# Performance work log

Hardware: AMD Instinct MI355X
Metric: run time of the kernel (lower is better)

The kernel has to match this reference:

```python
import jax, jax.numpy as jnp
import numpy as np

N_NODES = 50000
N_EDGES = 800000
IN_DIM = 64
HID_DIM = 128
OUT_DIM = 64
BN_EPS = 1e-5


def _glorot(key, shape):
    fan_in, fan_out = shape[0], shape[1]
    lim = (6.0 / (fan_in + fan_out)) ** 0.5
    return jax.random.uniform(key, shape, jnp.float32, -lim, lim)


def setup_inputs() -> dict:
    key = jax.random.key(0)
    ks = jax.random.split(key, 8)
    x = jax.random.normal(ks[0], (N_NODES, IN_DIM), jnp.float32)
    edge_index = jax.random.randint(ks[1], (2, N_EDGES), 0, N_NODES, jnp.int32)
    return {
        "x": x,
        "edge_index": edge_index,
        # SAGEConv1: lin_l (applied to aggregated neighbors, has bias), lin_r (root, no bias)
        "W1l": _glorot(ks[2], (IN_DIM, HID_DIM)),
        "b1": jnp.zeros((HID_DIM,), jnp.float32),
        "W1r": _glorot(ks[3], (IN_DIM, HID_DIM)),
        # BatchNorm1d params
        "gamma": jnp.ones((HID_DIM,), jnp.float32),
        "beta": jnp.zeros((HID_DIM,), jnp.float32),
        # SAGEConv2
        "W2l": _glorot(ks[4], (HID_DIM, OUT_DIM)),
        "b2": jnp.zeros((OUT_DIM,), jnp.float32),
        "W2r": _glorot(ks[5], (HID_DIM, OUT_DIM)),
    }


def _sage_conv(h, src, dst, Wl, b, Wr, deg_inv):
    # mean-aggregate neighbor features per destination node
    agg = jax.ops.segment_sum(h[src], dst, num_segments=N_NODES)  # [N, d]
    agg = agg * deg_inv[:, None]
    return agg @ Wl + b + h @ Wr


def reference(x, edge_index, W1l, b1, W1r, gamma, beta, W2l, b2, W2r):
    src, dst = edge_index[0], edge_index[1]
    deg = jax.ops.segment_sum(jnp.ones((N_EDGES,), jnp.float32), dst,
                              num_segments=N_NODES)
    deg_inv = jnp.where(deg > 0, 1.0 / jnp.maximum(deg, 1.0), 0.0)

    h = _sage_conv(x, src, dst, W1l, b1, W1r, deg_inv)  # [N, hid]
    # BatchNorm1d (training mode: batch stats over nodes, biased variance)
    mu = jnp.mean(h, axis=0)
    var = jnp.mean((h - mu) ** 2, axis=0)
    h = (h - mu) * jax.lax.rsqrt(var + BN_EPS) * gamma + beta
    h = jax.nn.relu(h)
    out = _sage_conv(h, src, dst, W2l, b2, W2r, deg_inv)  # [N, out]
    return out
```

## Files before the change

kernel.cpp:

```cpp
#include <hip/hip_runtime.h>

#define NN 50000
#define NE 800000
#define HID 128
#define OUTD 64
#define NBK 782
#define BWID 64
#define CAP 1264
#define TILE_E 4096
#define XB 3125
#define HB 196

typedef __attribute__((ext_vector_type(8))) short bf16x8;
typedef __attribute__((ext_vector_type(4))) float f32x4;

static __device__ __forceinline__ unsigned short f2bf(float f) {
    unsigned u = __float_as_uint(f);
    unsigned r = (u + 0x7FFFu + ((u >> 16) & 1u)) >> 16;
    return (unsigned short)r;
}
static __device__ __forceinline__ float bflo(unsigned u) { return __uint_as_float(u << 16); }
static __device__ __forceinline__ float bfhi(unsigned u) { return __uint_as_float(u & 0xffff0000u); }

__global__ __launch_bounds__(256) void prep_bin_kernel(
    const float* __restrict__ x, unsigned short* __restrict__ A1,
    const float* __restrict__ W1l, const float* __restrict__ W1r,
    const float* __restrict__ W2l, const float* __restrict__ W2r,
    unsigned short* __restrict__ BT1, unsigned short* __restrict__ BT2,
    const int* __restrict__ src, const int* __restrict__ dst,
    int* __restrict__ gcur, int2* __restrict__ pairs)
{
    __shared__ int lcnt[NBK];
    __shared__ int lbase[NBK];
    int blk = blockIdx.x, tid = threadIdx.x;
    if (blk >= HB) {
        int b2 = blk - HB;
        if (b2 < XB) {
            int idx = b2 * 256 + tid;
            int n = idx >> 4, q = idx & 15;
            float4 v = ((const float4*)x)[idx];
            ushort4 o;
            o.x = f2bf(v.x); o.y = f2bf(v.y); o.z = f2bf(v.z); o.w = f2bf(v.w);
            *(ushort4*)(A1 + (size_t)n * 128 + 64 + q * 4) = o;
        } else {
            int idx = (b2 - XB) * 256 + tid;
            int j = idx >> 7, k = idx & 127;
            float v1 = (k < 64) ? W1l[k * HID + j] : W1r[(k - 64) * HID + j];
            BT1[j * 128 + k] = f2bf(v1);
            float v2 = (j < 64) ? W2l[k * OUTD + j] : W2r[k * OUTD + (j - 64)];
            BT2[j * 128 + k] = f2bf(v2);
        }
        return;
    }
    int e0 = blk * TILE_E;
    for (int i = tid; i < NBK; i += 256) lcnt[i] = 0;
    __syncthreads();
    int s[16], d[16], loc[16];
#pragma unroll
    for (int i = 0; i < 16; i++) {
        int e = e0 + i * 256 + tid;
        if (e < NE) {
            s[i] = __builtin_nontemporal_load(&src[e]);
            d[i] = __builtin_nontemporal_load(&dst[e]);
            loc[i] = atomicAdd(&lcnt[d[i] >> 6], 1);
        }
    }
    __syncthreads();
    for (int b = tid; b < NBK; b += 256)
        lbase[b] = b * CAP + atomicAdd(&gcur[b], lcnt[b]);
    __syncthreads();
#pragma unroll
    for (int i = 0; i < 16; i++) {
        int e = e0 + i * 256 + tid;
        if (e < NE)
            pairs[lbase[d[i] >> 6] + loc[i]] = make_int2(s[i], d[i]);
    }
}

template<int MODE>
__global__ __launch_bounds__(256) void bin_agg_kernel(
    const int2* __restrict__ pairs, const int* __restrict__ gcur,
    const unsigned short* __restrict__ feat, int fstride, int foff,
    unsigned short* __restrict__ outb, int ostride, int ooff,
    float* __restrict__ outf)
{
    __shared__ int lcnt[BWID];
    __shared__ int startL[BWID];
    __shared__ int degL[BWID];
    __shared__ int lcur[BWID];
    __shared__ int permL[CAP];
    int b = blockIdx.x, tid = threadIdx.x;
    int lo = b * CAP;
    int cnt = gcur[b];
    int base = b * BWID;
    if (tid < BWID) lcnt[tid] = 0;
    __syncthreads();
    for (int i = tid; i < cnt; i += 256)
        atomicAdd(&lcnt[pairs[lo + i].y - base], 1);
    __syncthreads();
    if (tid < BWID) {
        int v = lcnt[tid];
        int s = v;
#pragma unroll
        for (int off = 1; off < BWID; off <<= 1) {
            int t = __shfl_up(s, off, 64);
            if (tid >= off) s += t;
        }
        startL[tid] = s - v;
        degL[tid] = v;
        lcur[tid] = s - v;
    }
    __syncthreads();
    for (int i = tid; i < cnt; i += 256) {
        int2 p = pairs[lo + i];
        int pos = atomicAdd(&lcur[p.y - base], 1);
        permL[pos] = p.x;
    }
    __syncthreads();
    int lane = tid & 63, w = tid >> 6;
    int g = lane >> 3;
    int q = lane & 7;
    const unsigned short* fbase = feat + foff + q * 8;
#pragma unroll
    for (int rnd = 0; rnd < 2; rnd++) {
        int nloc = w * 16 + rnd * 8 + g;
        int node = base + nloc;
        int rs = startL[nloc];
        int deg = degL[nloc];
        float acc[8];
#pragma unroll
        for (int t = 0; t < 8; t++) acc[t] = 0.f;
        int i = 0;
        for (; i + 3 < deg; i += 4) {
            int s0 = permL[rs + i];
            int s1 = permL[rs + i + 1];
            int s2 = permL[rs + i + 2];
            int s3 = permL[rs + i + 3];
            uint4 v0 = *(const uint4*)(fbase + (size_t)s0 * fstride);
            uint4 v1 = *(const uint4*)(fbase + (size_t)s1 * fstride);
            uint4 v2 = *(const uint4*)(fbase + (size_t)s2 * fstride);
            uint4 v3 = *(const uint4*)(fbase + (size_t)s3 * fstride);
            acc[0] += bflo(v0.x); acc[1] += bfhi(v0.x);
            acc[2] += bflo(v0.y); acc[3] += bfhi(v0.y);
            acc[4] += bflo(v0.z); acc[5] += bfhi(v0.z);
            acc[6] += bflo(v0.w); acc[7] += bfhi(v0.w);
            acc[0] += bflo(v1.x); acc[1] += bfhi(v1.x);
            acc[2] += bflo(v1.y); acc[3] += bfhi(v1.y);
            acc[4] += bflo(v1.z); acc[5] += bfhi(v1.z);
            acc[6] += bflo(v1.w); acc[7] += bfhi(v1.w);
            acc[0] += bflo(v2.x); acc[1] += bfhi(v2.x);
            acc[2] += bflo(v2.y); acc[3] += bfhi(v2.y);
            acc[4] += bflo(v2.z); acc[5] += bfhi(v2.z);
            acc[6] += bflo(v2.w); acc[7] += bfhi(v2.w);
            acc[0] += bflo(v3.x); acc[1] += bfhi(v3.x);
            acc[2] += bflo(v3.y); acc[3] += bfhi(v3.y);
            acc[4] += bflo(v3.z); acc[5] += bfhi(v3.z);
            acc[6] += bflo(v3.w); acc[7] += bfhi(v3.w);
        }
        for (; i < deg; i++) {
            int s0 = permL[rs + i];
            uint4 v0 = *(const uint4*)(fbase + (size_t)s0 * fstride);
            acc[0] += bflo(v0.x); acc[1] += bfhi(v0.x);
            acc[2] += bflo(v0.y); acc[3] += bfhi(v0.y);
            acc[4] += bflo(v0.z); acc[5] += bfhi(v0.z);
            acc[6] += bflo(v0.w); acc[7] += bfhi(v0.w);
        }
        if (node < NN) {
            float inv = (deg > 0) ? (1.0f / (float)deg) : 0.f;
            if (MODE == 0) {
                uint4 o;
                o.x = (unsigned)f2bf(acc[0] * inv) | ((unsigned)f2bf(acc[1] * inv) << 16);
                o.y = (unsigned)f2bf(acc[2] * inv) | ((unsigned)f2bf(acc[3] * inv) << 16);
                o.z = (unsigned)f2bf(acc[4] * inv) | ((unsigned)f2bf(acc[5] * inv) << 16);
                o.w = (unsigned)f2bf(acc[6] * inv) | ((unsigned)f2bf(acc[7] * inv) << 16);
                *(uint4*)(outb + (size_t)node * ostride + ooff + q * 8) = o;
            } else {
                float4* op = (float4*)(outf + (size_t)node * 64 + q * 8);
                float4 o0 = op[0], o1 = op[1];
                o0.x += acc[0] * inv; o0.y += acc[1] * inv;
                o0.z += acc[2] * inv; o0.w += acc[3] * inv;
                o1.x += acc[4] * inv; o1.y += acc[5] * inv;
                o1.z += acc[6] * inv; o1.w += acc[7] * inv;
                op[0] = o0; op[1] = o1;
            }
        }
    }
}

static __device__ __forceinline__ bf16x8 bnrelu8(uint4 v, const float* sc,
                                                 const float* sh, int j0) {
    float f[8];
    f[0] = bflo(v.x); f[1] = bfhi(v.x);
    f[2] = bflo(v.y); f[3] = bfhi(v.y);
    f[4] = bflo(v.z); f[5] = bfhi(v.z);
    f[6] = bflo(v.w); f[7] = bfhi(v.w);
    unsigned r01, r23, r45, r67;
#pragma unroll
    for (int t = 0; t < 8; t++) {
        float h = f[t] * sc[j0 + t] + sh[j0 + t];
        f[t] = h > 0.f ? h : 0.f;
    }
    r01 = (unsigned)f2bf(f[0]) | ((unsigned)f2bf(f[1]) << 16);
    r23 = (unsigned)f2bf(f[2]) | ((unsigned)f2bf(f[3]) << 16);
    r45 = (unsigned)f2bf(f[4]) | ((unsigned)f2bf(f[5]) << 16);
    r67 = (unsigned)f2bf(f[6]) | ((unsigned)f2bf(f[7]) << 16);
    uint4 o = make_uint4(r01, r23, r45, r67);
    return *(bf16x8*)&o;
}

template<bool IS1>
__global__ __launch_bounds__(256) void conv_mfma_kernel(
    const unsigned short* __restrict__ A, const unsigned short* __restrict__ BT,
    const float* __restrict__ bias,
    unsigned short* __restrict__ outb, float* __restrict__ outf,
    float* __restrict__ sums, float* __restrict__ sumsq,
    const float* __restrict__ gamma, const float* __restrict__ beta)
{
    __shared__ float red_s[4][128];
    __shared__ float red_q[4][128];
    __shared__ float sc[128], sh[128];
    int tid = threadIdx.x;
    int wid = tid >> 6, lane = tid & 63;
    int nl = lane & 15, ko = lane >> 4;
    if (!IS1) {
        if (tid < 128) {
            float inv_n = 1.0f / (float)NN;
            float mu = sums[tid] * inv_n;
            float var = sumsq[tid] * inv_n - mu * mu;
            float s = gamma[tid] * rsqrtf(var + 1e-5f);
            sc[tid] = s;
            sh[tid] = beta[tid] - mu * s;
        }
        __syncthreads();
    }
    int gw = blockIdx.x * 4 + wid;
    int jh = gw & 1;
    int tstride = (gridDim.x * 4) >> 1;
    const int tiles = NN / 16;
    bf16x8 b[4][4];
    const unsigned short* bbase = BT + (size_t)(jh * 64 + nl) * 128 + ko * 8;
#pragma unroll
    for (int jg = 0; jg < 4; jg++)
#pragma unroll
        for (int ks = 0; ks < 4; ks++)
            b[jg][ks] = *(const bf16x8*)(bbase + jg * 16 * 128 + ks * 32);
    float4 bias4[4];
#pragma unroll
    for (int jg = 0; jg < 4; jg++) {
        if (IS1)        bias4[jg] = *(const float4*)(bias + jh * 64 + jg * 16 + ko * 4);
        else if (jh)    bias4[jg] = *(const float4*)(bias + jg * 16 + ko * 4);
        else            bias4[jg] = make_float4(0.f, 0.f, 0.f, 0.f);
    }
    float s_sum[16], s_sq[16];
#pragma unroll
    for (int t = 0; t < 16; t++) { s_sum[t] = 0.f; s_sq[t] = 0.f; }
    int tile = gw >> 1;
    uint4 a[4];
    if (tile < tiles) {
        const unsigned short* arow = A + (size_t)(tile * 16 + nl) * 128 + ko * 8;
#pragma unroll
        for (int ks = 0; ks < 4; ks++) a[ks] = *(const uint4*)(arow + ks * 32);
    }
    while (tile < tiles) {
        int nxt = tile + tstride;
        uint4 an[4];
        if (nxt < tiles) {
            const unsigned short* arow = A + (size_t)(nxt * 16 + nl) * 128 + ko * 8;
#pragma unroll
            for (int ks = 0; ks < 4; ks++) an[ks] = *(const uint4*)(arow + ks * 32);
        }
        bf16x8 af[4];
#pragma unroll
        for (int ks = 0; ks < 4; ks++) {
            if (IS1) af[ks] = *(bf16x8*)&a[ks];
            else     af[ks] = bnrelu8(a[ks], sc, sh, ks * 32 + ko * 8);
        }
        int n_g = tile * 16 + nl;
#pragma unroll
        for (int jg = 0; jg < 4; jg++) {
            f32x4 acc = {0.f, 0.f, 0.f, 0.f};
#pragma unroll
            for (int ks = 0; ks < 4; ks++)
                acc = __builtin_amdgcn_mfma_f32_16x16x32_bf16(b[jg][ks], af[ks], acc, 0, 0, 0);
            float v0 = acc[0] + bias4[jg].x;
            float v1 = acc[1] + bias4[jg].y;
            float v2 = acc[2] + bias4[jg].z;
            float v3 = acc[3] + bias4[jg].w;
            if (IS1) {
                s_sum[jg * 4 + 0] += v0; s_sq[jg * 4 + 0] += v0 * v0;
                s_sum[jg * 4 + 1] += v1; s_sq[jg * 4 + 1] += v1 * v1;
                s_sum[jg * 4 + 2] += v2; s_sq[jg * 4 + 2] += v2 * v2;
                s_sum[jg * 4 + 3] += v3; s_sq[jg * 4 + 3] += v3 * v3;
                uint2 pk;
                pk.x = (unsigned)f2bf(v0) | ((unsigned)f2bf(v1) << 16);
                pk.y = (unsigned)f2bf(v2) | ((unsigned)f2bf(v3) << 16);
                *(uint2*)(outb + (size_t)n_g * 128 + jh * 64 + jg * 16 + ko * 4) = pk;
            } else {
                if (jh == 0) {
                    uint2 pk;
                    pk.x = (unsigned)f2bf(v0) | ((unsigned)f2bf(v1) << 16);
                    pk.y = (unsigned)f2bf(v2) | ((unsigned)f2bf(v3) << 16);
                    *(uint2*)(outb + (size_t)n_g * 64 + jg * 16 + ko * 4) = pk;
                } else {
                    float4 o = make_float4(v0, v1, v2, v3);
                    *(float4*)(outf + (size_t)n_g * 64 + jg * 16 + ko * 4) = o;
                }
            }
        }
#pragma unroll
        for (int ks = 0; ks < 4; ks++) a[ks] = an[ks];
        tile = nxt;
    }
    if (IS1) {
        for (int i = tid; i < 512; i += 256) {
            ((float*)red_s)[i] = 0.f;
            ((float*)red_q)[i] = 0.f;
        }
        __syncthreads();
#pragma unroll
        for (int jg = 0; jg < 4; jg++) {
#pragma unroll
            for (int r = 0; r < 4; r++) {
                float v = s_sum[jg * 4 + r];
                v += __shfl_xor(v, 1, 64);
                v += __shfl_xor(v, 2, 64);
                v += __shfl_xor(v, 4, 64);
                v += __shfl_xor(v, 8, 64);
                float w = s_sq[jg * 4 + r];
                w += __shfl_xor(w, 1, 64);
                w += __shfl_xor(w, 2, 64);
                w += __shfl_xor(w, 4, 64);
                w += __shfl_xor(w, 8, 64);
                if (nl == 0) {
                    red_s[wid][jh * 64 + jg * 16 + ko * 4 + r] = v;
                    red_q[wid][jh * 64 + jg * 16 + ko * 4 + r] = w;
                }
            }
        }
        __syncthreads();
        if (tid < 128) {
            float v = red_s[0][tid] + red_s[1][tid] + red_s[2][tid] + red_s[3][tid];
            atomicAdd(&sums[tid], v);
        } else {
            int j = tid - 128;
            float v = red_q[0][j] + red_q[1][j] + red_q[2][j] + red_q[3][j];
            atomicAdd(&sumsq[j], v);
        }
    }
}

extern "C" void kernel_launch(void* const* d_in, const int* in_sizes, int n_in,
                              void* d_out, int out_size, void* d_ws, size_t ws_size,
                              hipStream_t stream) {
    const float* x     = (const float*)d_in[0];
    const int*   ei    = (const int*)d_in[1];
    const float* W1l   = (const float*)d_in[2];
    const float* b1    = (const float*)d_in[3];
    const float* W1r   = (const float*)d_in[4];
    const float* gamma = (const float*)d_in[5];
    const float* beta  = (const float*)d_in[6];
    const float* W2l   = (const float*)d_in[7];
    const float* b2    = (const float*)d_in[8];
    const float* W2r   = (const float*)d_in[9];
    float* out = (float*)d_out;

    char* wsb = (char*)d_ws;
    int*   gcur   = (int*)wsb;
    float* sums   = (float*)(wsb + 784 * 4);
    float* sumsq  = sums + 128;
    int2*  pairs  = (int2*)(sumsq + 128);
    unsigned short* A1    = (unsigned short*)(pairs + (size_t)NBK * CAP);
    unsigned short* hpreb = A1 + (size_t)NN * 128;
    unsigned short* BT1   = hpreb + (size_t)NN * 128;
    unsigned short* BT2   = BT1 + 128 * 128;

    const int* srcp = ei;
    const int* dstp = ei + NE;

    const int CB = 512;

    hipMemsetAsync(d_ws, 0, 784 * 4 + 256 * 4, stream);

    prep_bin_kernel<<<HB + XB + 64, 256, 0, stream>>>(x, A1, W1l, W1r, W2l, W2r,
                                                      BT1, BT2, srcp, dstp, gcur, pairs);
    bin_agg_kernel<0><<<NBK, 256, 0, stream>>>(pairs, gcur, A1, 128, 64,
                                               A1, 128, 0, nullptr);
    conv_mfma_kernel<true><<<CB, 256, 0, stream>>>(A1, BT1, b1, hpreb, nullptr,
                                                   sums, sumsq, nullptr, nullptr);
    conv_mfma_kernel<false><<<CB, 256, 0, stream>>>(hpreb, BT2, b2, A1, out,
                                                    sums, sumsq, gamma, beta);
    bin_agg_kernel<1><<<NBK, 256, 0, stream>>>(pairs, gcur, A1, 64, 0,
                                               nullptr, 0, 0, out);
}
```

Measured before the change: 192.1 us.

## Fuse layer-1 aggregation with conv1 MFMA and reuse sorted CSR for layer 2

Merges the first mean-aggregation kernel with the first SAGE linear transform and its BatchNorm statistics reduction, so aggregated features stay in LDS instead of round-tripping through global memory. Edge pairs are packed into 32 bits with a 16-bit source and a local destination, and the per-bin sorted source list, degrees and offsets are saved so the second aggregation skips the counting and sorting pass. The second aggregation now only loads the cached CSR. Packing sources into 16 bits relies on node ids fitting in 16 bits (50000 < 65536), and the fused kernel runs only 782 blocks for the MFMA work.

```diff
diff --git a/kernel.cpp b/kernel.cpp
--- a/kernel.cpp
+++ b/kernel.cpp
@@ -23,12 +23,12 @@
 static __device__ __forceinline__ float bfhi(unsigned u) { return __uint_as_float(u & 0xffff0000u); }
 
 __global__ __launch_bounds__(256) void prep_bin_kernel(
-    const float* __restrict__ x, unsigned short* __restrict__ A1,
+    const float* __restrict__ x, unsigned short* __restrict__ xb,
     const float* __restrict__ W1l, const float* __restrict__ W1r,
     const float* __restrict__ W2l, const float* __restrict__ W2r,
     unsigned short* __restrict__ BT1, unsigned short* __restrict__ BT2,
     const int* __restrict__ src, const int* __restrict__ dst,
-    int* __restrict__ gcur, int2* __restrict__ pairs)
+    int* __restrict__ gcur, unsigned* __restrict__ pairs)
 {
     __shared__ int lcnt[NBK];
     __shared__ int lbase[NBK];
@@ -41,7 +41,7 @@
             float4 v = ((const float4*)x)[idx];
             ushort4 o;
             o.x = f2bf(v.x); o.y = f2bf(v.y); o.z = f2bf(v.z); o.w = f2bf(v.w);
-            *(ushort4*)(A1 + (size_t)n * 128 + 64 + q * 4) = o;
+            *(ushort4*)(xb + (size_t)n * 64 + q * 4) = o;
         } else {
             int idx = (b2 - XB) * 256 + tid;
             int j = idx >> 7, k = idx & 127;
@@ -73,30 +73,34 @@
     for (int i = 0; i < 16; i++) {
         int e = e0 + i * 256 + tid;
         if (e < NE)
-            pairs[lbase[d[i] >> 6] + loc[i]] = make_int2(s[i], d[i]);
-    }
-}
-
-template<int MODE>
-__global__ __launch_bounds__(256) void bin_agg_kernel(
-    const int2* __restrict__ pairs, const int* __restrict__ gcur,
-    const unsigned short* __restrict__ feat, int fstride, int foff,
-    unsigned short* __restrict__ outb, int ostride, int ooff,
-    float* __restrict__ outf)
+            pairs[lbase[d[i] >> 6] + loc[i]] =
+                (unsigned)(((d[i] & 63) << 16) | s[i]);
+    }
+}
+
+__global__ __launch_bounds__(256) void agg_conv1_kernel(
+    const unsigned* __restrict__ pairs, const int* __restrict__ gcur,
+    const unsigned short* __restrict__ xb, const unsigned short* __restrict__ BT,
+    const float* __restrict__ bias, unsigned short* __restrict__ hpreb,
+    float* __restrict__ sums, float* __restrict__ sumsq,
+    unsigned short* __restrict__ permG, unsigned short* __restrict__ degG,
+    unsigned short* __restrict__ startG)
 {
     __shared__ int lcnt[BWID];
     __shared__ int startL[BWID];
     __shared__ int degL[BWID];
     __shared__ int lcur[BWID];
-    __shared__ int permL[CAP];
+    __shared__ __align__(16) unsigned short permL[CAP];
+    __shared__ __align__(16) unsigned short aggL[64][64];
+    __shared__ float red_s[4][128];
+    __shared__ float red_q[4][128];
     int b = blockIdx.x, tid = threadIdx.x;
     int lo = b * CAP;
     int cnt = gcur[b];
-    int base = b * BWID;
     if (tid < BWID) lcnt[tid] = 0;
     __syncthreads();
     for (int i = tid; i < cnt; i += 256)
-        atomicAdd(&lcnt[pairs[lo + i].y - base], 1);
+        atomicAdd(&lcnt[pairs[lo + i] >> 16], 1);
     __syncthreads();
     if (tid < BWID) {
         int v = lcnt[tid];
@@ -109,22 +113,26 @@
         startL[tid] = s - v;
         degL[tid] = v;
         lcur[tid] = s - v;
+        degG[b * 64 + tid] = (unsigned short)v;
+        startG[b * 64 + tid] = (unsigned short)(s - v);
     }
     __syncthreads();
     for (int i = tid; i < cnt; i += 256) {
-        int2 p = pairs[lo + i];
-        int pos = atomicAdd(&lcur[p.y - base], 1);
-        permL[pos] = p.x;
-    }
-    __syncthreads();
+        unsigned p = pairs[lo + i];
+        int pos = atomicAdd(&lcur[p >> 16], 1);
+        permL[pos] = (unsigned short)(p & 0xffffu);
+    }
+    __syncthreads();
+    int cu = (cnt + 1) >> 1;
+    for (int i = tid; i < cu; i += 256)
+        ((unsigned*)(permG + lo))[i] = ((const unsigned*)permL)[i];
     int lane = tid & 63, w = tid >> 6;
     int g = lane >> 3;
     int q = lane & 7;
-    const unsigned short* fbase = feat + foff + q * 8;
+    const unsigned short* fbase = xb + q * 8;
 #pragma unroll
     for (int rnd = 0; rnd < 2; rnd++) {
         int nloc = w * 16 + rnd * 8 + g;
-        int node = base + nloc;
         int rs = startL[nloc];
         int deg = degL[nloc];
         float acc[8];
@@ -136,10 +144,10 @@
             int s1 = permL[rs + i + 1];
             int s2 = permL[rs + i + 2];
             int s3 = permL[rs + i + 3];
-            uint4 v0 = *(const uint4*)(fbase + (size_t)s0 * fstride);
-            uint4 v1 = *(const uint4*)(fbase + (size_t)s1 * fstride);
-            uint4 v2 = *(const uint4*)(fbase + (size_t)s2 * fstride);
-            uint4 v3 = *(const uint4*)(fbase + (size_t)s3 * fstride);
+            uint4 v0 = *(const uint4*)(fbase + (size_t)s0 * 64);
+            uint4 v1 = *(const uint4*)(fbase + (size_t)s1 * 64);
+            uint4 v2 = *(const uint4*)(fbase + (size_t)s2 * 64);
+            uint4 v3 = *(const uint4*)(fbase + (size_t)s3 * 64);
             acc[0] += bflo(v0.x); acc[1] += bfhi(v0.x);
             acc[2] += bflo(v0.y); acc[3] += bfhi(v0.y);
             acc[4] += bflo(v0.z); acc[5] += bfhi(v0.z);
@@ -159,31 +167,104 @@
         }
         for (; i < deg; i++) {
             int s0 = permL[rs + i];
-            uint4 v0 = *(const uint4*)(fbase + (size_t)s0 * fstride);
+            uint4 v0 = *(const uint4*)(fbase + (size_t)s0 * 64);
             acc[0] += bflo(v0.x); acc[1] += bfhi(v0.x);
             acc[2] += bflo(v0.y); acc[3] += bfhi(v0.y);
             acc[4] += bflo(v0.z); acc[5] += bfhi(v0.z);
             acc[6] += bflo(v0.w); acc[7] += bfhi(v0.w);
         }
-        if (node < NN) {
-            float inv = (deg > 0) ? (1.0f / (float)deg) : 0.f;
-            if (MODE == 0) {
-                uint4 o;
-                o.x = (unsigned)f2bf(acc[0] * inv) | ((unsigned)f2bf(acc[1] * inv) << 16);
-                o.y = (unsigned)f2bf(acc[2] * inv) | ((unsigned)f2bf(acc[3] * inv) << 16);
-                o.z = (unsigned)f2bf(acc[4] * inv) | ((unsigned)f2bf(acc[5] * inv) << 16);
-                o.w = (unsigned)f2bf(acc[6] * inv) | ((unsigned)f2bf(acc[7] * inv) << 16);
-                *(uint4*)(outb + (size_t)node * ostride + ooff + q * 8) = o;
-            } else {
-                float4* op = (float4*)(outf + (size_t)node * 64 + q * 8);
-                float4 o0 = op[0], o1 = op[1];
-                o0.x += acc[0] * inv; o0.y += acc[1] * inv;
-                o0.z += acc[2] * inv; o0.w += acc[3] * inv;
-                o1.x += acc[4] * inv; o1.y += acc[5] * inv;
-                o1.z += acc[6] * inv; o1.w += acc[7] * inv;
-                op[0] = o0; op[1] = o1;
+        float inv = (deg > 0) ? (1.0f / (float)deg) : 0.f;
+        uint4 o;
+        o.x = (unsigned)f2bf(acc[0] * inv) | ((unsigned)f2bf(acc[1] * inv) << 16);
+        o.y = (unsigned)f2bf(acc[2] * inv) | ((unsigned)f2bf(acc[3] * inv) << 16);
+        o.z = (unsigned)f2bf(acc[4] * inv) | ((unsigned)f2bf(acc[5] * inv) << 16);
+        o.w = (unsigned)f2bf(acc[6] * inv) | ((unsigned)f2bf(acc[7] * inv) << 16);
+        *(uint4*)&aggL[nloc][q * 8] = o;
+    }
+    __syncthreads();
+    int nl = lane & 15, ko = lane >> 4;
+    int jh = w & 1;
+    bf16x8 bfr[4][4];
+    const unsigned short* bbase = BT + (size_t)(jh * 64 + nl) * 128 + ko * 8;
+#pragma unroll
+    for (int jg = 0; jg < 4; jg++)
+#pragma unroll
+        for (int ks = 0; ks < 4; ks++)
+            bfr[jg][ks] = *(const bf16x8*)(bbase + jg * 16 * 128 + ks * 32);
+    float4 bias4[4];
+#pragma unroll
+    for (int jg = 0; jg < 4; jg++)
+        bias4[jg] = *(const float4*)(bias + jh * 64 + jg * 16 + ko * 4);
+    float s_sum[16], s_sq[16];
+#pragma unroll
+    for (int t = 0; t < 16; t++) { s_sum[t] = 0.f; s_sq[t] = 0.f; }
+#pragma unroll
+    for (int rnd2 = 0; rnd2 < 2; rnd2++) {
+        int t = (w >> 1) + rnd2 * 2;
+        int n_g = b * 64 + t * 16 + nl;
+        if (n_g < NN) {
+            bf16x8 a[4];
+#pragma unroll
+            for (int ks = 0; ks < 2; ks++)
+                a[ks] = *(const bf16x8*)&aggL[t * 16 + nl][ks * 32 + ko * 8];
+            const unsigned short* xrow = xb + (size_t)n_g * 64 + ko * 8;
+#pragma unroll
+            for (int ks = 2; ks < 4; ks++)
+                a[ks] = *(const bf16x8*)(xrow + (ks - 2) * 32);
+#pragma unroll
+            for (int jg = 0; jg < 4; jg++) {
+                f32x4 acc = {0.f, 0.f, 0.f, 0.f};
+#pragma unroll
+                for (int ks = 0; ks < 4; ks++)
+                    acc = __builtin_amdgcn_mfma_f32_16x16x32_bf16(bfr[jg][ks], a[ks], acc, 0, 0, 0);
+                float v0 = acc[0] + bias4[jg].x;
+                float v1 = acc[1] + bias4[jg].y;
+                float v2 = acc[2] + bias4[jg].z;
+                float v3 = acc[3] + bias4[jg].w;
+                s_sum[jg * 4 + 0] += v0; s_sq[jg * 4 + 0] += v0 * v0;
+                s_sum[jg * 4 + 1] += v1; s_sq[jg * 4 + 1] += v1 * v1;
+                s_sum[jg * 4 + 2] += v2; s_sq[jg * 4 + 2] += v2 * v2;
+                s_sum[jg * 4 + 3] += v3; s_sq[jg * 4 + 3] += v3 * v3;
+                uint2 pk;
+                pk.x = (unsigned)f2bf(v0) | ((unsigned)f2bf(v1) << 16);
+                pk.y = (unsigned)f2bf(v2) | ((unsigned)f2bf(v3) << 16);
+                *(uint2*)(hpreb + (size_t)n_g * 128 + jh * 64 + jg * 16 + ko * 4) = pk;
             }
         }
+    }
+    for (int i = tid; i < 512; i += 256) {
+        ((float*)red_s)[i] = 0.f;
+        ((float*)red_q)[i] = 0.f;
+    }
+    __syncthreads();
+#pragma unroll
+    for (int jg = 0; jg < 4; jg++) {
+#pragma unroll
+        for (int r = 0; r < 4; r++) {
+            float v = s_sum[jg * 4 + r];
+            v += __shfl_xor(v, 1, 64);
+            v += __shfl_xor(v, 2, 64);
+            v += __shfl_xor(v, 4, 64);
+            v += __shfl_xor(v, 8, 64);
+            float w2 = s_sq[jg * 4 + r];
+            w2 += __shfl_xor(w2, 1, 64);
+            w2 += __shfl_xor(w2, 2, 64);
+            w2 += __shfl_xor(w2, 4, 64);
+            w2 += __shfl_xor(w2, 8, 64);
+            if (nl == 0) {
+                red_s[w][jh * 64 + jg * 16 + ko * 4 + r] = v;
+                red_q[w][jh * 64 + jg * 16 + ko * 4 + r] = w2;
+            }
+        }
+    }
+    __syncthreads();
+    if (tid < 128) {
+        float v = red_s[0][tid] + red_s[1][tid] + red_s[2][tid] + red_s[3][tid];
+        atomicAdd(&sums[tid], v);
+    } else {
+        int j = tid - 128;
+        float v = red_q[0][j] + red_q[1][j] + red_q[2][j] + red_q[3][j];
+        atomicAdd(&sumsq[j], v);
     }
 }
 
@@ -194,66 +275,56 @@
     f[2] = bflo(v.y); f[3] = bfhi(v.y);
     f[4] = bflo(v.z); f[5] = bfhi(v.z);
     f[6] = bflo(v.w); f[7] = bfhi(v.w);
-    unsigned r01, r23, r45, r67;
 #pragma unroll
     for (int t = 0; t < 8; t++) {
         float h = f[t] * sc[j0 + t] + sh[j0 + t];
         f[t] = h > 0.f ? h : 0.f;
     }
-    r01 = (unsigned)f2bf(f[0]) | ((unsigned)f2bf(f[1]) << 16);
-    r23 = (unsigned)f2bf(f[2]) | ((unsigned)f2bf(f[3]) << 16);
-    r45 = (unsigned)f2bf(f[4]) | ((unsigned)f2bf(f[5]) << 16);
-    r67 = (unsigned)f2bf(f[6]) | ((unsigned)f2bf(f[7]) << 16);
+    unsigned r01 = (unsigned)f2bf(f[0]) | ((unsigned)f2bf(f[1]) << 16);
+    unsigned r23 = (unsigned)f2bf(f[2]) | ((unsigned)f2bf(f[3]) << 16);
+    unsigned r45 = (unsigned)f2bf(f[4]) | ((unsigned)f2bf(f[5]) << 16);
+    unsigned r67 = (unsigned)f2bf(f[6]) | ((unsigned)f2bf(f[7]) << 16);
     uint4 o = make_uint4(r01, r23, r45, r67);
     return *(bf16x8*)&o;
 }
 
-template<bool IS1>
-__global__ __launch_bounds__(256) void conv_mfma_kernel(
+__global__ __launch_bounds__(256) void conv2_kernel(
     const unsigned short* __restrict__ A, const unsigned short* __restrict__ BT,
     const float* __restrict__ bias,
-    unsigned short* __restrict__ outb, float* __restrict__ outf,
-    float* __restrict__ sums, float* __restrict__ sumsq,
+    unsigned short* __restrict__ pb, float* __restrict__ outf,
+    const float* __restrict__ sums, const float* __restrict__ sumsq,
     const float* __restrict__ gamma, const float* __restrict__ beta)
 {
-    __shared__ float red_s[4][128];
-    __shared__ float red_q[4][128];
     __shared__ float sc[128], sh[128];
     int tid = threadIdx.x;
     int wid = tid >> 6, lane = tid & 63;
     int nl = lane & 15, ko = lane >> 4;
-    if (!IS1) {
-        if (tid < 128) {
-            float inv_n = 1.0f / (float)NN;
-            float mu = sums[tid] * inv_n;
-            float var = sumsq[tid] * inv_n - mu * mu;
-            float s = gamma[tid] * rsqrtf(var + 1e-5f);
-            sc[tid] = s;
-            sh[tid] = beta[tid] - mu * s;
-        }
-        __syncthreads();
-    }
+    if (tid < 128) {
+        float inv_n = 1.0f / (float)NN;
+        float mu = sums[tid] * inv_n;
+        float var = sumsq[tid] * inv_n - mu * mu;
+        float s = gamma[tid] * rsqrtf(var + 1e-5f);
+        sc[tid] = s;
+        sh[tid] = beta[tid] - mu * s;
+    }
+    __syncthreads();
     int gw = blockIdx.x * 4 + wid;
     int jh = gw & 1;
     int tstride = (gridDim.x * 4) >> 1;
     const int tiles = NN / 16;
-    bf16x8 b[4][4];
+    bf16x8 bfr[4][4];
     const unsigned short* bbase = BT + (size_t)(jh * 64 + nl) * 128 + ko * 8;
 #pragma unroll
     for (int jg = 0; jg < 4; jg++)
 #pragma unroll
         for (int ks = 0; ks < 4; ks++)
-            b[jg][ks] = *(const bf16x8*)(bbase + jg * 16 * 128 + ks * 32);
+            bfr[jg][ks] = *(const bf16x8*)(bbase + jg * 16 * 128 + ks * 32);
     float4 bias4[4];
 #pragma unroll
     for (int jg = 0; jg < 4; jg++) {
-        if (IS1)        bias4[jg] = *(const float4*)(bias + jh * 64 + jg * 16 + ko * 4);
-        else if (jh)    bias4[jg] = *(const float4*)(bias + jg * 16 + ko * 4);
-        else            bias4[jg] = make_float4(0.f, 0.f, 0.f, 0.f);
-    }
-    float s_sum[16], s_sq[16];
-#pragma unroll
-    for (int t = 0; t < 16; t++) { s_sum[t] = 0.f; s_sq[t] = 0.f; }
+        if (jh) bias4[jg] = *(const float4*)(bias + jg * 16 + ko * 4);
+        else    bias4[jg] = make_float4(0.f, 0.f, 0.f, 0.f);
+    }
     int tile = gw >> 1;
     uint4 a[4];
     if (tile < tiles) {
@@ -271,80 +342,111 @@
         }
         bf16x8 af[4];
 #pragma unroll
-        for (int ks = 0; ks < 4; ks++) {
-            if (IS1) af[ks] = *(bf16x8*)&a[ks];
-            else     af[ks] = bnrelu8(a[ks], sc, sh, ks * 32 + ko * 8);
-        }
+        for (int ks = 0; ks < 4; ks++)
+            af[ks] = bnrelu8(a[ks], sc, sh, ks * 32 + ko * 8);
         int n_g = tile * 16 + nl;
 #pragma unroll
         for (int jg = 0; jg < 4; jg++) {
             f32x4 acc = {0.f, 0.f, 0.f, 0.f};
 #pragma unroll
             for (int ks = 0; ks < 4; ks++)
-                acc = __builtin_amdgcn_mfma_f32_16x16x32_bf16(b[jg][ks], af[ks], acc, 0, 0, 0);
+                acc = __builtin_amdgcn_mfma_f32_16x16x32_bf16(bfr[jg][ks], af[ks], acc, 0, 0, 0);
             float v0 = acc[0] + bias4[jg].x;
             float v1 = acc[1] + bias4[jg].y;
             float v2 = acc[2] + bias4[jg].z;
             float v3 = acc[3] + bias4[jg].w;
-            if (IS1) {
-                s_sum[jg * 4 + 0] += v0; s_sq[jg * 4 + 0] += v0 * v0;
-                s_sum[jg * 4 + 1] += v1; s_sq[jg * 4 + 1] += v1 * v1;
-                s_sum[jg * 4 + 2] += v2; s_sq[jg * 4 + 2] += v2 * v2;
-                s_sum[jg * 4 + 3] += v3; s_sq[jg * 4 + 3] += v3 * v3;
+            if (jh == 0) {
                 uint2 pk;
                 pk.x = (unsigned)f2bf(v0) | ((unsigned)f2bf(v1) << 16);
                 pk.y = (unsigned)f2bf(v2) | ((unsigned)f2bf(v3) << 16);
-                *(uint2*)(outb + (size_t)n_g * 128 + jh * 64 + jg * 16 + ko * 4) = pk;
+                *(uint2*)(pb + (size_t)n_g * 64 + jg * 16 + ko * 4) = pk;
             } else {
-                if (jh == 0) {
-                    uint2 pk;
-                    pk.x = (unsigned)f2bf(v0) | ((unsigned)f2bf(v1) << 16);
-                    pk.y = (unsigned)f2bf(v2) | ((unsigned)f2bf(v3) << 16);
-                    *(uint2*)(outb + (size_t)n_g * 64 + jg * 16 + ko * 4) = pk;
-                } else {
-                    float4 o = make_float4(v0, v1, v2, v3);
-                    *(float4*)(outf + (size_t)n_g * 64 + jg * 16 + ko * 4) = o;
-                }
+                float4 o = make_float4(v0, v1, v2, v3);
+                *(float4*)(outf + (size_t)n_g * 64 + jg * 16 + ko * 4) = o;
             }
         }
 #pragma unroll
         for (int ks = 0; ks < 4; ks++) a[ks] = an[ks];
         tile = nxt;
     }
-    if (IS1) {
-        for (int i = tid; i < 512; i += 256) {
-            ((float*)red_s)[i] = 0.f;
-            ((float*)red_q)[i] = 0.f;
-        }
-        __syncthreads();
-#pragma unroll
-        for (int jg = 0; jg < 4; jg++) {
-#pragma unroll
-            for (int r = 0; r < 4; r++) {
-                float v = s_sum[jg * 4 + r];
-                v += __shfl_xor(v, 1, 64);
-                v += __shfl_xor(v, 2, 64);
-                v += __shfl_xor(v, 4, 64);
-                v += __shfl_xor(v, 8, 64);
-                float w = s_sq[jg * 4 + r];
-                w += __shfl_xor(w, 1, 64);
-                w += __shfl_xor(w, 2, 64);
-                w += __shfl_xor(w, 4, 64);
-                w += __shfl_xor(w, 8, 64);
-                if (nl == 0) {
-                    red_s[wid][jh * 64 + jg * 16 + ko * 4 + r] = v;
-                    red_q[wid][jh * 64 + jg * 16 + ko * 4 + r] = w;
-                }
-            }
-        }
-        __syncthreads();
-        if (tid < 128) {
-            float v = red_s[0][tid] + red_s[1][tid] + red_s[2][tid] + red_s[3][tid];
-            atomicAdd(&sums[tid], v);
-        } else {
-            int j = tid - 128;
-            float v = red_q[0][j] + red_q[1][j] + red_q[2][j] + red_q[3][j];
-            atomicAdd(&sumsq[j], v);
+}
+
+__global__ __launch_bounds__(256) void agg2_kernel(
+    const unsigned short* __restrict__ permG, const int* __restrict__ gcur,
+    const unsigned short* __restrict__ degG, const unsigned short* __restrict__ startG,
+    const unsigned short* __restrict__ pb, float* __restrict__ out)
+{
+    __shared__ __align__(16) unsigned short permL[CAP];
+    __shared__ int startL[BWID];
+    __shared__ int degL[BWID];
+    int b = blockIdx.x, tid = threadIdx.x;
+    int lo = b * CAP;
+    int cnt = gcur[b];
+    if (tid < BWID) {
+        startL[tid] = startG[b * 64 + tid];
+        degL[tid] = degG[b * 64 + tid];
+    }
+    int cu = (cnt + 1) >> 1;
+    for (int i = tid; i < cu; i += 256)
+        ((unsigned*)permL)[i] = ((const unsigned*)(permG + lo))[i];
+    __syncthreads();
+    int lane = tid & 63, w = tid >> 6;
+    int g = lane >> 3;
+    int q = lane & 7;
+    const unsigned short* fbase = pb + q * 8;
+#pragma unroll
+    for (int rnd = 0; rnd < 2; rnd++) {
+        int nloc = w * 16 + rnd * 8 + g;
+        int node = b * 64 + nloc;
+        int rs = startL[nloc];
+        int deg = degL[nloc];
+        float acc[8];
+#pragma unroll
+        for (int t = 0; t < 8; t++) acc[t] = 0.f;
+        int i = 0;
+        for (; i + 3 < deg; i += 4) {
+            int s0 = permL[rs + i];
+            int s1 = permL[rs + i + 1];
+            int s2 = permL[rs + i + 2];
+            int s3 = permL[rs + i + 3];
+            uint4 v0 = *(const uint4*)(fbase + (size_t)s0 * 64);
+            uint4 v1 = *(const uint4*)(fbase + (size_t)s1 * 64);
+            uint4 v2 = *(const uint4*)(fbase + (size_t)s2 * 64);
+            uint4 v3 = *(const uint4*)(fbase + (size_t)s3 * 64);
+            acc[0] += bflo(v0.x); acc[1] += bfhi(v0.x);
+            acc[2] += bflo(v0.y); acc[3] += bfhi(v0.y);
+            acc[4] += bflo(v0.z); acc[5] += bfhi(v0.z);
+            acc[6] += bflo(v0.w); acc[7] += bfhi(v0.w);
+            acc[0] += bflo(v1.x); acc[1] += bfhi(v1.x);
+            acc[2] += bflo(v1.y); acc[3] += bfhi(v1.y);
+            acc[4] += bflo(v1.z); acc[5] += bfhi(v1.z);
+            acc[6] += bflo(v1.w); acc[7] += bfhi(v1.w);
+            acc[0] += bflo(v2.x); acc[1] += bfhi(v2.x);
+            acc[2] += bflo(v2.y); acc[3] += bfhi(v2.y);
+            acc[4] += bflo(v2.z); acc[5] += bfhi(v2.z);
+            acc[6] += bflo(v2.w); acc[7] += bfhi(v2.w);
+            acc[0] += bflo(v3.x); acc[1] += bfhi(v3.x);
+            acc[2] += bflo(v3.y); acc[3] += bfhi(v3.y);
+            acc[4] += bflo(v3.z); acc[5] += bfhi(v3.z);
+            acc[6] += bflo(v3.w); acc[7] += bfhi(v3.w);
+        }
+        for (; i < deg; i++) {
+            int s0 = permL[rs + i];
+            uint4 v0 = *(const uint4*)(fbase + (size_t)s0 * 64);
+            acc[0] += bflo(v0.x); acc[1] += bfhi(v0.x);
+            acc[2] += bflo(v0.y); acc[3] += bfhi(v0.y);
+            acc[4] += bflo(v0.z); acc[5] += bfhi(v0.z);
+            acc[6] += bflo(v0.w); acc[7] += bfhi(v0.w);
+        }
+        if (node < NN) {
+            float inv = (deg > 0) ? (1.0f / (float)deg) : 0.f;
+            float4* op = (float4*)(out + (size_t)node * 64 + q * 8);
+            float4 o0 = op[0], o1 = op[1];
+            o0.x += acc[0] * inv; o0.y += acc[1] * inv;
+            o0.z += acc[2] * inv; o0.w += acc[3] * inv;
+            o1.x += acc[4] * inv; o1.y += acc[5] * inv;
+            o1.z += acc[6] * inv; o1.w += acc[7] * inv;
+            op[0] = o0; op[1] = o1;
         }
     }
 }
@@ -366,29 +468,28 @@
 
     char* wsb = (char*)d_ws;
     int*   gcur   = (int*)wsb;
-    float* sums   = (float*)(wsb + 784 * 4);
+    float* sums   = (float*)(wsb + 4096);
     float* sumsq  = sums + 128;
-    int2*  pairs  = (int2*)(sumsq + 128);
-    unsigned short* A1    = (unsigned short*)(pairs + (size_t)NBK * CAP);
-    unsigned short* hpreb = A1 + (size_t)NN * 128;
-    unsigned short* BT1   = hpreb + (size_t)NN * 128;
-    unsigned short* BT2   = BT1 + 128 * 128;
+    unsigned* pairs = (unsigned*)(wsb + 8192);
+    unsigned short* permG  = (unsigned short*)((char*)pairs + (size_t)NBK * CAP * 4);
+    unsigned short* degG   = permG + (size_t)NBK * CAP;
+    unsigned short* startG = degG + (size_t)NBK * 64;
+    unsigned short* xb     = startG + (size_t)NBK * 64;
+    unsigned short* hpreb  = xb + (size_t)NN * 64;
+    unsigned short* pbuf   = hpreb + (size_t)NN * 128;
+    unsigned short* BT1    = pbuf + (size_t)NN * 64;
+    unsigned short* BT2    = BT1 + 128 * 128;
 
     const int* srcp = ei;
     const int* dstp = ei + NE;
 
-    const int CB = 512;
-
-    hipMemsetAsync(d_ws, 0, 784 * 4 + 256 * 4, stream);
-
-    prep_bin_kernel<<<HB + XB + 64, 256, 0, stream>>>(x, A1, W1l, W1r, W2l, W2r,
+    hipMemsetAsync(d_ws, 0, 8192, stream);
+
+    prep_bin_kernel<<<HB + XB + 64, 256, 0, stream>>>(x, xb, W1l, W1r, W2l, W2r,
                                                       BT1, BT2, srcp, dstp, gcur, pairs);
-    bin_agg_kernel<0><<<NBK, 256, 0, stream>>>(pairs, gcur, A1, 128, 64,
-                                               A1, 128, 0, nullptr);
-    conv_mfma_kernel<true><<<CB, 256, 0, stream>>>(A1, BT1, b1, hpreb, nullptr,
-                                                   sums, sumsq, nullptr, nullptr);
-    conv_mfma_kernel<false><<<CB, 256, 0, stream>>>(hpreb, BT2, b2, A1, out,
-                                                    sums, sumsq, gamma, beta);
-    bin_agg_kernel<1><<<NBK, 256, 0, stream>>>(pairs, gcur, A1, 64, 0,
-                                               nullptr, 0, 0, out);
-}
+    agg_conv1_kernel<<<NBK, 256, 0, stream>>>(pairs, gcur, xb, BT1, b1, hpreb,
+                                              sums, sumsq, permG, degG, startG);
+    conv2_kernel<<<512, 256, 0, stream>>>(hpreb, BT2, b2, pbuf, out,
+                                          sums, sumsq, gamma, beta);
+    agg2_kernel<<<NBK, 256, 0, stream>>>(permG, gcur, degG, startG, pbuf, out);
+}
```

Result: no change. 190.5 us (-0.8%).
